# Performance work log

Measured on AMD Instinct MI355X. Metric: run time of the kernel, lower is better.

The kernel has to match this reference:

```python
import jax, jax.numpy as jnp
import numpy as np

EMBED = 1024
HEADS = 16
HEAD_DIM = EMBED // HEADS
LN_EPS = 1e-5


def setup_inputs() -> dict:
    key = jax.random.key(0)
    ks = jax.random.split(key, 12)
    B, LQ, LK = 2, 2048, 2048
    s = 1.0 / np.sqrt(EMBED)
    inp = {
        "query_seq": jax.random.normal(ks[0], (B, LQ, EMBED), jnp.float32),
        "key_value_seq": jax.random.normal(ks[1], (B, LK, EMBED), jnp.float32),
        "prompt_size": 0,
        "Wq": jax.random.normal(ks[2], (EMBED, EMBED), jnp.float32) * s,
        "bq": jnp.zeros((EMBED,), jnp.float32),
        "Wk": jax.random.normal(ks[3], (EMBED, EMBED), jnp.float32) * s,
        "bk": jnp.zeros((EMBED,), jnp.float32),
        "Wv": jax.random.normal(ks[4], (EMBED, EMBED), jnp.float32) * s,
        "bv": jnp.zeros((EMBED,), jnp.float32),
        "Wo": jax.random.normal(ks[5], (EMBED, EMBED), jnp.float32) * s,
        "bo": jnp.zeros((EMBED,), jnp.float32),
        "ln_gamma": jnp.ones((EMBED,), jnp.float32),
        "ln_beta": jnp.zeros((EMBED,), jnp.float32),
    }
    return inp


def _split_heads(x):
    B, L, _ = x.shape
    return x.reshape(B, L, HEADS, HEAD_DIM).transpose(0, 2, 1, 3)  # [B,H,L,Dh]


def reference(query_seq, key_value_seq, prompt_size, Wq, bq, Wk, bk, Wv, bv, Wo, bo, ln_gamma, ln_beta):
    # projections (torch nn.Linear: x @ W.T + b)
    q = _split_heads(query_seq @ Wq.T + bq)
    k = _split_heads(key_value_seq @ Wk.T + bk)
    v = _split_heads(key_value_seq @ Wv.T + bv)
    # naive attention: full score matrix, softmax over keys
    scores = jnp.einsum("bhqd,bhkd->bhqk", q, k) / np.sqrt(HEAD_DIM).astype(np.float32)
    attn = jax.nn.softmax(scores, axis=-1)
    ctx = jnp.einsum("bhqk,bhkd->bhqd", attn, v)
    B, H, LQ, Dh = ctx.shape
    ctx = ctx.transpose(0, 2, 1, 3).reshape(B, LQ, H * Dh)
    out = ctx @ Wo.T + bo
    # residual + LayerNorm
    x = out + query_seq
    mu = jnp.mean(x, axis=-1, keepdims=True)
    var = jnp.var(x, axis=-1, keepdims=True)
    return (x - mu) * jax.lax.rsqrt(var + LN_EPS) * ln_gamma + ln_beta
```

## Files before the change

kernel.cpp:

```cpp
#include <hip/hip_runtime.h>

typedef unsigned short u16;
typedef unsigned int u32;
typedef __attribute__((ext_vector_type(8))) __bf16 bf16x8;
typedef __attribute__((ext_vector_type(4))) short short4v;
typedef __attribute__((ext_vector_type(4))) float f32x4;
typedef __attribute__((ext_vector_type(16))) float f32x16;

#define EMBED 1024
#define NB 2
#define LQ 2048
#define HEADS 16
#define DH 64
#define QSCALE 0.18033688011112042f

__device__ __forceinline__ u16 f2bf(float f) {
  u32 u = __float_as_uint(f);
  u32 r = (u + 0x7FFFu + ((u >> 16) & 1u)) >> 16;
  return (u16)r;
}

__device__ __forceinline__ void glds16(const void* g, void* l) {
  __builtin_amdgcn_global_load_lds((const __attribute__((address_space(1))) void*)g,
                                   (__attribute__((address_space(3))) void*)l, 16, 0, 0);
}

__device__ __forceinline__ f32x4 mfma16(bf16x8 a, bf16x8 b, f32x4 c) {
  return __builtin_amdgcn_mfma_f32_16x16x32_bf16(a, b, c, 0, 0, 0);
}
__device__ __forceinline__ f32x16 mfma32(bf16x8 a, bf16x8 b, f32x16 c) {
  return __builtin_amdgcn_mfma_f32_32x32x16_bf16(a, b, c, 0, 0, 0);
}
__device__ __forceinline__ f32x16 mfma32x8(short4v a, short4v b, f32x16 c) {
  return __builtin_amdgcn_mfma_f32_32x32x8bf16_1k(a, b, c, 0, 0, 0);
}

__device__ __forceinline__ u32 packbf(float a, float b) {
  return __builtin_amdgcn_perm(__float_as_uint(b), __float_as_uint(a), 0x07060302u);
}

__global__ __launch_bounds__(256) void cast_kernel(
    const float* __restrict__ q, const float* __restrict__ kv,
    const float* __restrict__ wq, const float* __restrict__ wk,
    const float* __restrict__ wv, const float* __restrict__ wo,
    u16* __restrict__ qb, u16* __restrict__ kvb, u16* __restrict__ wqb,
    u16* __restrict__ wkb, u16* __restrict__ wvb, u16* __restrict__ wob) {
  int bid = blockIdx.x;
  const float* src;
  u16* dst;
  long base;
  if (bid < 2048) {
    src = q; dst = qb; base = (long)bid * 2048;
  } else if (bid < 4096) {
    src = kv; dst = kvb; base = (long)(bid - 2048) * 2048;
  } else {
    int wsel = (bid - 4096) >> 9;
    int wb = (bid - 4096) & 511;
    if (wsel == 0) { src = wq; dst = wqb; }
    else if (wsel == 1) { src = wk; dst = wkb; }
    else if (wsel == 2) { src = wv; dst = wvb; }
    else { src = wo; dst = wob; }
    base = (long)wb * 2048;
  }
  long e = base + (long)threadIdx.x * 8;
  float4 f0 = *(const float4*)(src + e);
  float4 f1 = *(const float4*)(src + e + 4);
  uint4 o;
  o.x = (u32)f2bf(f0.x) | ((u32)f2bf(f0.y) << 16);
  o.y = (u32)f2bf(f0.z) | ((u32)f2bf(f0.w) << 16);
  o.z = (u32)f2bf(f1.x) | ((u32)f2bf(f1.y) << 16);
  o.w = (u32)f2bf(f1.z) | ((u32)f2bf(f1.w) << 16);
  *(uint4*)(dst + e) = o;
}

template <int IT>
__device__ __forceinline__ void gemm_core(
    u16* As, u16* Bs, const u16* __restrict__ A, const u16* __restrict__ W,
    const float* __restrict__ bias, const float* __restrict__ resid,
    void* __restrict__ outp, int mode, int bx, int by) {
  const int K = EMBED;
  const int TM = IT * 32;
  const int tid = threadIdx.x;
  const int lane = tid & 63;
  const int wv = tid >> 6;
  const int wm = wv >> 1, wn = wv & 1;
  const int l16 = lane & 15, quad = lane >> 4;
  const long tile_m = (long)bx * TM;
  const long tile_n = (long)by * 128;

  f32x4 z4 = {0.f, 0.f, 0.f, 0.f};
  f32x4 acc[IT][4];
#pragma unroll
  for (int i = 0; i < IT; i++)
#pragma unroll
    for (int j = 0; j < 4; j++) acc[i][j] = z4;

  for (int k0 = 0; k0 < K; k0 += 64) {
#pragma unroll
    for (int it = 0; it < TM / 32; it++) {
      int lin = it * 256 + tid;
      int row = lin >> 3, cc = lin & 7;
      glds16(A + (tile_m + row) * K + k0 + ((cc ^ (row & 7)) << 3), As + lin * 8);
    }
#pragma unroll
    for (int it = 0; it < 4; it++) {
      int lin = it * 256 + tid;
      int row = lin >> 3, cc = lin & 7;
      glds16(W + (tile_n + row) * K + k0 + ((cc ^ (row & 7)) << 3), Bs + lin * 8);
    }
    __syncthreads();
    bf16x8 af[IT][2], bfr[4][2];
#pragma unroll
    for (int i = 0; i < IT; i++) {
      int row = wm * (IT * 16) + i * 16 + l16;
#pragma unroll
      for (int ki = 0; ki < 2; ki++)
        af[i][ki] = *(const bf16x8*)(As + row * 64 + (((ki * 4 + quad) ^ (row & 7)) << 3));
    }
#pragma unroll
    for (int j = 0; j < 4; j++) {
      int row = wn * 64 + j * 16 + l16;
#pragma unroll
      for (int ki = 0; ki < 2; ki++)
        bfr[j][ki] = *(const bf16x8*)(Bs + row * 64 + (((ki * 4 + quad) ^ (row & 7)) << 3));
    }
#pragma unroll
    for (int ki = 0; ki < 2; ki++)
#pragma unroll
      for (int i = 0; i < IT; i++)
#pragma unroll
        for (int j = 0; j < 4; j++) acc[i][j] = mfma16(af[i][ki], bfr[j][ki], acc[i][j]);
    __syncthreads();
  }

#pragma unroll
  for (int j = 0; j < 4; j++) {
    int gn = (int)tile_n + wn * 64 + j * 16 + l16;
    float bv = bias[gn];
#pragma unroll
    for (int i = 0; i < IT; i++) {
      long gm0 = tile_m + wm * (IT * 16) + i * 16 + quad * 4;
      if (mode == 3) {
#pragma unroll
        for (int r = 0; r < 4; r++) {
          long idx = (gm0 + r) * EMBED + gn;
          ((float*)outp)[idx] = acc[i][j][r] + bv + resid[idx];
        }
      } else if (mode == 2) {
        int b = (int)(gm0 >> 11), l = (int)(gm0 & 2047);
        int hh = gn >> 6, dh = gn & 63;
        uint2 pk;
        pk.x = (u32)f2bf(acc[i][j][0] + bv) | ((u32)f2bf(acc[i][j][1] + bv) << 16);
        pk.y = (u32)f2bf(acc[i][j][2] + bv) | ((u32)f2bf(acc[i][j][3] + bv) << 16);
        *(uint2*)((u16*)outp + (long)((b * HEADS + hh) * DH + dh) * LQ + l) = pk;
      } else {
#pragma unroll
        for (int r = 0; r < 4; r++) {
          long gm = gm0 + r;
          float v = acc[i][j][r] + bv;
          if (mode == 0) v *= QSCALE;
          int b = (int)(gm >> 11), l = (int)(gm & 2047);
          int hh = gn >> 6, dh = gn & 63;
          ((u16*)outp)[(long)((b * HEADS + hh) * LQ + l) * DH + dh] = f2bf(v);
        }
      }
    }
  }
}

__global__ __launch_bounds__(256) void qkv_kernel(
    const u16* __restrict__ qb, const u16* __restrict__ kvb,
    const u16* __restrict__ wqb, const u16* __restrict__ wkb, const u16* __restrict__ wvb,
    const float* __restrict__ bq, const float* __restrict__ bk, const float* __restrict__ bv,
    u16* __restrict__ Qh, u16* __restrict__ Kh, u16* __restrict__ Vt) {
  __shared__ u16 As[128 * 64];
  __shared__ u16 Bs[128 * 64];
  if (blockIdx.z == 0)      gemm_core<4>(As, Bs, qb,  wqb, bq, nullptr, Qh, 0, blockIdx.x, blockIdx.y);
  else if (blockIdx.z == 1) gemm_core<4>(As, Bs, kvb, wkb, bk, nullptr, Kh, 1, blockIdx.x, blockIdx.y);
  else                      gemm_core<4>(As, Bs, kvb, wvb, bv, nullptr, Vt, 2, blockIdx.x, blockIdx.y);
}

__global__ __launch_bounds__(256) void oproj_kernel(
    const u16* __restrict__ ctx, const u16* __restrict__ wob,
    const float* __restrict__ bo, const float* __restrict__ resid, float* __restrict__ out) {
  __shared__ u16 As[64 * 64];
  __shared__ u16 Bs[128 * 64];
  gemm_core<2>(As, Bs, ctx, wob, bo, resid, out, 3, blockIdx.x, blockIdx.y);
}

__global__ __launch_bounds__(256, 2) void attn_kernel(
    const u16* __restrict__ Qh, const u16* __restrict__ Kh,
    const u16* __restrict__ Vt, u16* __restrict__ ctx) {
  __shared__ u16 Qs[128 * 64];
  __shared__ u16 KVs[2][2][64 * 64];
  const int tid = threadIdx.x;
  const int lane = tid & 63;
  const int wv = tid >> 6;
  const int l32 = lane & 31, h = lane >> 5;
  const int qt = blockIdx.x, bh = blockIdx.y;
  const long qoff = (long)bh * (LQ * DH) + (long)qt * (128 * DH);
  const long koff = (long)bh * (LQ * DH);
  const long voff = (long)bh * (DH * LQ);
  const int qbase = wv * 32;

#pragma unroll
  for (int it = 0; it < 4; it++) {
    int lin = it * 256 + tid;
    int row = lin >> 3, cc = lin & 7;
    glds16(Qh + qoff + row * 64 + ((cc ^ (row & 7)) << 3), Qs + lin * 8);
  }
#pragma unroll
  for (int it = 0; it < 2; it++) {
    int lin = it * 256 + tid;
    int row = lin >> 3, cc = lin & 7;
    glds16(Kh + koff + (long)row * 64 + ((cc ^ (row & 7)) << 3), KVs[0][0] + lin * 8);
    glds16(Vt + voff + (long)row * LQ + ((cc ^ (row & 7)) << 3), KVs[0][1] + lin * 8);
  }
  __syncthreads();

  bf16x8 bq[4];
  {
    int row = qbase + l32;
#pragma unroll
    for (int ks = 0; ks < 4; ks++)
      bq[ks] = *(const bf16x8*)(Qs + row * 64 + (((ks * 2 + h) ^ (row & 7)) << 3));
  }

  f32x16 z16 = {0.f, 0.f, 0.f, 0.f, 0.f, 0.f, 0.f, 0.f,
                0.f, 0.f, 0.f, 0.f, 0.f, 0.f, 0.f, 0.f};
  f32x16 ot[2];
  ot[0] = z16;
  ot[1] = z16;
  float2 ls2 = {0.f, 0.f};

  for (int kt = 0; kt < 32; kt++) {
    const u16* Ks = KVs[kt & 1][0];
    const u16* Vts = KVs[kt & 1][1];
    if (kt + 1 < 32) {
      u16* Kn = (u16*)KVs[(kt + 1) & 1][0];
      u16* Vn = (u16*)KVs[(kt + 1) & 1][1];
#pragma unroll
      for (int it = 0; it < 2; it++) {
        int lin = it * 256 + tid;
        int row = lin >> 3, cc = lin & 7;
        glds16(Kh + koff + (long)((kt + 1) * 64 + row) * 64 + ((cc ^ (row & 7)) << 3), Kn + lin * 8);
        glds16(Vt + voff + (long)row * LQ + (kt + 1) * 64 + ((cc ^ (row & 7)) << 3), Vn + lin * 8);
      }
    }

    f32x16 st[2];
    st[0] = z16;
    st[1] = z16;
#pragma unroll
    for (int ks = 0; ks < 4; ks++) {
#pragma unroll
      for (int mt = 0; mt < 2; mt++) {
        int row = mt * 32 + l32;
        bf16x8 ak = *(const bf16x8*)(Ks + row * 64 + (((ks * 2 + h) ^ (row & 7)) << 3));
        st[mt] = mfma32(ak, bq[ks], st[mt]);
      }
    }

    uint2 pk[2][4];
#pragma unroll
    for (int mt = 0; mt < 2; mt++) {
#pragma unroll
      for (int g = 0; g < 4; g++) {
        float p0 = exp2f(st[mt][g * 4 + 0]);
        float p1 = exp2f(st[mt][g * 4 + 1]);
        float p2 = exp2f(st[mt][g * 4 + 2]);
        float p3 = exp2f(st[mt][g * 4 + 3]);
        float2 a = {p0, p1}, bb = {p2, p3};
        ls2.x += a.x + bb.x;
        ls2.y += a.y + bb.y;
        pk[mt][g].x = packbf(p0, p1);
        pk[mt][g].y = packbf(p2, p3);
      }
    }

#pragma unroll
    for (int t = 0; t < 8; t++) {
      short4v bp = *(short4v*)&pk[t >> 2][t & 3];
#pragma unroll
      for (int mt2 = 0; mt2 < 2; mt2++) {
        int row = mt2 * 32 + l32;
        short4v av = *(const short4v*)(Vts + row * 64 + (((t ^ (row & 7))) << 3) + 4 * h);
        ot[mt2] = mfma32x8(av, bp, ot[mt2]);
      }
    }
    __syncthreads();
  }

  float lsum = ls2.x + ls2.y;
  lsum += __shfl_xor(lsum, 32);
  float inv = 1.0f / lsum;

  const int b = bh >> 4, head = bh & 15;
  int qrow = qt * 128 + qbase + l32;
  long base = (long)(b * LQ + qrow) * EMBED + head * DH;
#pragma unroll
  for (int mt = 0; mt < 2; mt++) {
#pragma unroll
    for (int g = 0; g < 4; g++) {
      uint2 pkk;
      pkk.x = (u32)f2bf(ot[mt][g * 4 + 0] * inv) | ((u32)f2bf(ot[mt][g * 4 + 1] * inv) << 16);
      pkk.y = (u32)f2bf(ot[mt][g * 4 + 2] * inv) | ((u32)f2bf(ot[mt][g * 4 + 3] * inv) << 16);
      *(uint2*)(ctx + base + mt * 32 + g * 8 + 4 * h) = pkk;
    }
  }
}

__global__ __launch_bounds__(256) void ln_kernel(
    float* __restrict__ x, const float* __restrict__ gamma, const float* __restrict__ beta) {
  __shared__ float red[8];
  const int tid = threadIdx.x;
  const long row = blockIdx.x;
  float4 v = *(const float4*)(x + row * EMBED + tid * 4);
  float s = v.x + v.y + v.z + v.w;
  float sq = v.x * v.x + v.y * v.y + v.z * v.z + v.w * v.w;
#pragma unroll
  for (int off = 1; off < 64; off <<= 1) {
    s += __shfl_xor(s, off);
    sq += __shfl_xor(sq, off);
  }
  if ((tid & 63) == 0) {
    red[(tid >> 6) * 2] = s;
    red[(tid >> 6) * 2 + 1] = sq;
  }
  __syncthreads();
  s = red[0] + red[2] + red[4] + red[6];
  sq = red[1] + red[3] + red[5] + red[7];
  float mu = s * (1.f / EMBED);
  float var = sq * (1.f / EMBED) - mu * mu;
  float rstd = rsqrtf(var + 1e-5f);
  float4 g = *(const float4*)(gamma + tid * 4);
  float4 bt = *(const float4*)(beta + tid * 4);
  float4 ov;
  ov.x = (v.x - mu) * rstd * g.x + bt.x;
  ov.y = (v.y - mu) * rstd * g.y + bt.y;
  ov.z = (v.z - mu) * rstd * g.z + bt.z;
  ov.w = (v.w - mu) * rstd * g.w + bt.w;
  *(float4*)(x + row * EMBED + tid * 4) = ov;
}

extern "C" void kernel_launch(void* const* d_in, const int* in_sizes, int n_in,
                              void* d_out, int out_size, void* d_ws, size_t ws_size,
                              hipStream_t stream) {
  const float* q     = (const float*)d_in[0];
  const float* kv    = (const float*)d_in[1];
  const float* Wq    = (const float*)d_in[3];
  const float* bq    = (const float*)d_in[4];
  const float* Wk    = (const float*)d_in[5];
  const float* bk    = (const float*)d_in[6];
  const float* Wv    = (const float*)d_in[7];
  const float* bv    = (const float*)d_in[8];
  const float* Wo    = (const float*)d_in[9];
  const float* bo    = (const float*)d_in[10];
  const float* gamma = (const float*)d_in[11];
  const float* beta  = (const float*)d_in[12];

  char* ws = (char*)d_ws;
  u16* qb  = (u16*)(ws + (0l  << 20));
  u16* kvb = (u16*)(ws + (8l  << 20));
  u16* wqb = (u16*)(ws + (16l << 20));
  u16* wkb = (u16*)(ws + (18l << 20));
  u16* wvb = (u16*)(ws + (20l << 20));
  u16* wob = (u16*)(ws + (22l << 20));
  u16* Qh  = (u16*)(ws + (24l << 20));
  u16* Kh  = (u16*)(ws + (32l << 20));
  u16* Vt  = (u16*)(ws + (40l << 20));
  u16* ctx = (u16*)(ws + (48l << 20));
  float* out = (float*)d_out;

  cast_kernel<<<6144, 256, 0, stream>>>(q, kv, Wq, Wk, Wv, Wo, qb, kvb, wqb, wkb, wvb, wob);
  qkv_kernel<<<dim3(32, 8, 3), 256, 0, stream>>>(qb, kvb, wqb, wkb, wvb, bq, bk, bv, Qh, Kh, Vt);
  attn_kernel<<<dim3(16, 32), 256, 0, stream>>>(Qh, Kh, Vt, ctx);
  oproj_kernel<<<dim3(64, 8), 256, 0, stream>>>(ctx, wob, bo, q, out);
  ln_kernel<<<4096, 256, 0, stream>>>(out, gamma, beta);
}
```

Measured before the change: 241.6 us.

## Software-pipeline attention loop with triple-buffered KV and 32x32x16 PV MFMA

Restructures the attention main loop so the softmax of tile k-1 and its PV product run interleaved with the QK^T MFMAs for tile k, backed by a third KV LDS buffer and a two-tile prefetch distance. The PV step switches from the 32x32x8 MFMA to the 32x32x16 variant, using v_permlane32_swap to rearrange the packed probabilities into the wider operand layout. It also adds s_setprio around the MFMA blocks. The aim is to hide exp/convert latency and global-load latency behind matrix work and to halve the number of PV MFMA issues, at the cost of more LDS per block (occupancy risk with launch_bounds 256,2) and more live registers.

```diff
diff --git a/kernel.cpp b/kernel.cpp
--- a/kernel.cpp
+++ b/kernel.cpp
@@ -3,7 +3,6 @@
 typedef unsigned short u16;
 typedef unsigned int u32;
 typedef __attribute__((ext_vector_type(8))) __bf16 bf16x8;
-typedef __attribute__((ext_vector_type(4))) short short4v;
 typedef __attribute__((ext_vector_type(4))) float f32x4;
 typedef __attribute__((ext_vector_type(16))) float f32x16;
 
@@ -31,8 +30,9 @@
 __device__ __forceinline__ f32x16 mfma32(bf16x8 a, bf16x8 b, f32x16 c) {
   return __builtin_amdgcn_mfma_f32_32x32x16_bf16(a, b, c, 0, 0, 0);
 }
-__device__ __forceinline__ f32x16 mfma32x8(short4v a, short4v b, f32x16 c) {
-  return __builtin_amdgcn_mfma_f32_32x32x8bf16_1k(a, b, c, 0, 0, 0);
+
+__device__ __forceinline__ void pl32(u32& a, u32& b) {
+  asm("v_permlane32_swap_b32 %0, %1" : "+v"(a), "+v"(b));
 }
 
 __device__ __forceinline__ u32 packbf(float a, float b) {
@@ -192,7 +192,7 @@
     const u16* __restrict__ Qh, const u16* __restrict__ Kh,
     const u16* __restrict__ Vt, u16* __restrict__ ctx) {
   __shared__ u16 Qs[128 * 64];
-  __shared__ u16 KVs[2][2][64 * 64];
+  __shared__ u16 KVs[3][2][64 * 64];
   const int tid = threadIdx.x;
   const int lane = tid & 63;
   const int wv = tid >> 6;
@@ -203,19 +203,26 @@
   const long voff = (long)bh * (DH * LQ);
   const int qbase = wv * 32;
 
+  auto stage_kv = [&](int t, int r) {
+    u16* Kn = (u16*)KVs[r][0];
+    u16* Vn = (u16*)KVs[r][1];
+#pragma unroll
+    for (int it = 0; it < 2; it++) {
+      int lin = it * 256 + tid;
+      int row = lin >> 3, cc = lin & 7;
+      glds16(Kh + koff + (long)(t * 64 + row) * 64 + ((cc ^ (row & 7)) << 3), Kn + lin * 8);
+      glds16(Vt + voff + (long)row * LQ + t * 64 + ((cc ^ (row & 7)) << 3), Vn + lin * 8);
+    }
+  };
+
 #pragma unroll
   for (int it = 0; it < 4; it++) {
     int lin = it * 256 + tid;
     int row = lin >> 3, cc = lin & 7;
     glds16(Qh + qoff + row * 64 + ((cc ^ (row & 7)) << 3), Qs + lin * 8);
   }
-#pragma unroll
-  for (int it = 0; it < 2; it++) {
-    int lin = it * 256 + tid;
-    int row = lin >> 3, cc = lin & 7;
-    glds16(Kh + koff + (long)row * 64 + ((cc ^ (row & 7)) << 3), KVs[0][0] + lin * 8);
-    glds16(Vt + voff + (long)row * LQ + ((cc ^ (row & 7)) << 3), KVs[0][1] + lin * 8);
-  }
+  stage_kv(0, 0);
+  stage_kv(1, 1);
   __syncthreads();
 
   bf16x8 bq[4];
@@ -231,26 +238,14 @@
   f32x16 ot[2];
   ot[0] = z16;
   ot[1] = z16;
+  f32x16 st[2];
+  uint2 pk[2][4];
   float2 ls2 = {0.f, 0.f};
 
-  for (int kt = 0; kt < 32; kt++) {
-    const u16* Ks = KVs[kt & 1][0];
-    const u16* Vts = KVs[kt & 1][1];
-    if (kt + 1 < 32) {
-      u16* Kn = (u16*)KVs[(kt + 1) & 1][0];
-      u16* Vn = (u16*)KVs[(kt + 1) & 1][1];
-#pragma unroll
-      for (int it = 0; it < 2; it++) {
-        int lin = it * 256 + tid;
-        int row = lin >> 3, cc = lin & 7;
-        glds16(Kh + koff + (long)((kt + 1) * 64 + row) * 64 + ((cc ^ (row & 7)) << 3), Kn + lin * 8);
-        glds16(Vt + voff + (long)row * LQ + (kt + 1) * 64 + ((cc ^ (row & 7)) << 3), Vn + lin * 8);
-      }
-    }
-
-    f32x16 st[2];
+  auto do_S = [&](const u16* Ks) {
     st[0] = z16;
     st[1] = z16;
+    __builtin_amdgcn_s_setprio(1);
 #pragma unroll
     for (int ks = 0; ks < 4; ks++) {
 #pragma unroll
@@ -260,8 +255,10 @@
         st[mt] = mfma32(ak, bq[ks], st[mt]);
       }
     }
-
-    uint2 pk[2][4];
+    __builtin_amdgcn_s_setprio(0);
+  };
+
+  auto do_softmax = [&]() {
 #pragma unroll
     for (int mt = 0; mt < 2; mt++) {
 #pragma unroll
@@ -270,26 +267,53 @@
         float p1 = exp2f(st[mt][g * 4 + 1]);
         float p2 = exp2f(st[mt][g * 4 + 2]);
         float p3 = exp2f(st[mt][g * 4 + 3]);
-        float2 a = {p0, p1}, bb = {p2, p3};
-        ls2.x += a.x + bb.x;
-        ls2.y += a.y + bb.y;
+        ls2.x += p0 + p2;
+        ls2.y += p1 + p3;
         pk[mt][g].x = packbf(p0, p1);
         pk[mt][g].y = packbf(p2, p3);
       }
     }
-
-#pragma unroll
-    for (int t = 0; t < 8; t++) {
-      short4v bp = *(short4v*)&pk[t >> 2][t & 3];
+  };
+
+  auto do_PV = [&](const u16* Vts) {
+#pragma unroll
+    for (int s = 0; s < 4; s++) {
+      uint2 wa = pk[s >> 1][(s & 1) * 2];
+      uint2 wb = pk[s >> 1][(s & 1) * 2 + 1];
+      u32 a0 = wa.x, b0 = wb.x, a1 = wa.y, b1 = wb.y;
+      pl32(a0, b0);
+      pl32(a1, b1);
+      union { u32 u[4]; bf16x8 v; } bp;
+      bp.u[0] = a0;
+      bp.u[1] = a1;
+      bp.u[2] = b0;
+      bp.u[3] = b1;
+      __builtin_amdgcn_s_setprio(1);
 #pragma unroll
       for (int mt2 = 0; mt2 < 2; mt2++) {
         int row = mt2 * 32 + l32;
-        short4v av = *(const short4v*)(Vts + row * 64 + (((t ^ (row & 7))) << 3) + 4 * h);
-        ot[mt2] = mfma32x8(av, bp, ot[mt2]);
+        bf16x8 av = *(const bf16x8*)(Vts + row * 64 + ((((s << 1) + h) ^ (row & 7)) << 3));
+        ot[mt2] = mfma32(av, bp.v, ot[mt2]);
       }
-    }
+      __builtin_amdgcn_s_setprio(0);
+    }
+  };
+
+  do_S(KVs[0][0]);
+
+  int prv = 0, cur = 1, nxt = 2;
+  for (int kt = 1; kt < 32; kt++) {
+    if (kt + 1 < 32) stage_kv(kt + 1, nxt);
+    do_softmax();
+    do_S(KVs[cur][0]);
+    do_PV(KVs[prv][1]);
     __syncthreads();
-  }
+    prv = cur;
+    cur = nxt;
+    nxt = (nxt == 2) ? 0 : nxt + 1;
+  }
+  do_softmax();
+  do_PV(KVs[prv][1]);
 
   float lsum = ls2.x + ls2.y;
   lsum += __shfl_xor(lsum, 32);
```

New measurement: 234.5 us. -2.9%, faster.

## Software-pipeline attention loop with triple-buffered KV and wider PV MFMA

Applied to the files above, without the earlier changes.

The attention inner loop is restructured so each iteration runs the softmax of the previous tile, the QK^T MFMAs of the current tile and the PV MFMAs of the previous tile. K/V tiles are staged two ahead into a third LDS buffer. The PV product switches from the 32x32x8 MFMA to 32x32x16 by regrouping the probability registers with v_permlane32_swap, and s_setprio is raised around the MFMA blocks. The goal is to overlap exp/pack work with matrix ops and halve the PV MFMA count. The cost is more LDS per block and more live registers.

```diff
diff --git a/kernel.cpp b/kernel.cpp
--- a/kernel.cpp
+++ b/kernel.cpp
@@ -3,7 +3,6 @@
 typedef unsigned short u16;
 typedef unsigned int u32;
 typedef __attribute__((ext_vector_type(8))) __bf16 bf16x8;
-typedef __attribute__((ext_vector_type(4))) short short4v;
 typedef __attribute__((ext_vector_type(4))) float f32x4;
 typedef __attribute__((ext_vector_type(16))) float f32x16;
 
@@ -31,8 +30,9 @@
 __device__ __forceinline__ f32x16 mfma32(bf16x8 a, bf16x8 b, f32x16 c) {
   return __builtin_amdgcn_mfma_f32_32x32x16_bf16(a, b, c, 0, 0, 0);
 }
-__device__ __forceinline__ f32x16 mfma32x8(short4v a, short4v b, f32x16 c) {
-  return __builtin_amdgcn_mfma_f32_32x32x8bf16_1k(a, b, c, 0, 0, 0);
+
+__device__ __forceinline__ void pl32(u32& a, u32& b) {
+  asm("v_permlane32_swap_b32 %0, %1" : "+v"(a), "+v"(b));
 }
 
 __device__ __forceinline__ u32 packbf(float a, float b) {
@@ -192,7 +192,7 @@
     const u16* __restrict__ Qh, const u16* __restrict__ Kh,
     const u16* __restrict__ Vt, u16* __restrict__ ctx) {
   __shared__ u16 Qs[128 * 64];
-  __shared__ u16 KVs[2][2][64 * 64];
+  __shared__ u16 KVs[3][2][64 * 64];
   const int tid = threadIdx.x;
   const int lane = tid & 63;
   const int wv = tid >> 6;
@@ -203,19 +203,26 @@
   const long voff = (long)bh * (DH * LQ);
   const int qbase = wv * 32;
 
+#define STAGE_KV(t, N)                                                          \
+  do {                                                                          \
+    _Pragma("unroll") for (int it = 0; it < 2; it++) {                          \
+      int lin = it * 256 + tid;                                                 \
+      int row = lin >> 3, cc = lin & 7;                                         \
+      glds16(Kh + koff + (long)((t) * 64 + row) * 64 + ((cc ^ (row & 7)) << 3), \
+             &KVs[N][0][0] + lin * 8);                                          \
+      glds16(Vt + voff + (long)row * LQ + (t) * 64 + ((cc ^ (row & 7)) << 3),   \
+             &KVs[N][1][0] + lin * 8);                                          \
+    }                                                                           \
+  } while (0)
+
 #pragma unroll
   for (int it = 0; it < 4; it++) {
     int lin = it * 256 + tid;
     int row = lin >> 3, cc = lin & 7;
     glds16(Qh + qoff + row * 64 + ((cc ^ (row & 7)) << 3), Qs + lin * 8);
   }
-#pragma unroll
-  for (int it = 0; it < 2; it++) {
-    int lin = it * 256 + tid;
-    int row = lin >> 3, cc = lin & 7;
-    glds16(Kh + koff + (long)row * 64 + ((cc ^ (row & 7)) << 3), KVs[0][0] + lin * 8);
-    glds16(Vt + voff + (long)row * LQ + ((cc ^ (row & 7)) << 3), KVs[0][1] + lin * 8);
-  }
+  STAGE_KV(0, 0);
+  STAGE_KV(1, 1);
   __syncthreads();
 
   bf16x8 bq[4];
@@ -231,65 +238,91 @@
   f32x16 ot[2];
   ot[0] = z16;
   ot[1] = z16;
+  f32x16 st[2];
+  uint2 pk[2][4];
   float2 ls2 = {0.f, 0.f};
 
-  for (int kt = 0; kt < 32; kt++) {
-    const u16* Ks = KVs[kt & 1][0];
-    const u16* Vts = KVs[kt & 1][1];
-    if (kt + 1 < 32) {
-      u16* Kn = (u16*)KVs[(kt + 1) & 1][0];
-      u16* Vn = (u16*)KVs[(kt + 1) & 1][1];
-#pragma unroll
-      for (int it = 0; it < 2; it++) {
-        int lin = it * 256 + tid;
-        int row = lin >> 3, cc = lin & 7;
-        glds16(Kh + koff + (long)((kt + 1) * 64 + row) * 64 + ((cc ^ (row & 7)) << 3), Kn + lin * 8);
-        glds16(Vt + voff + (long)row * LQ + (kt + 1) * 64 + ((cc ^ (row & 7)) << 3), Vn + lin * 8);
-      }
-    }
-
-    f32x16 st[2];
-    st[0] = z16;
-    st[1] = z16;
-#pragma unroll
-    for (int ks = 0; ks < 4; ks++) {
-#pragma unroll
-      for (int mt = 0; mt < 2; mt++) {
-        int row = mt * 32 + l32;
-        bf16x8 ak = *(const bf16x8*)(Ks + row * 64 + (((ks * 2 + h) ^ (row & 7)) << 3));
-        st[mt] = mfma32(ak, bq[ks], st[mt]);
-      }
-    }
-
-    uint2 pk[2][4];
-#pragma unroll
-    for (int mt = 0; mt < 2; mt++) {
-#pragma unroll
-      for (int g = 0; g < 4; g++) {
-        float p0 = exp2f(st[mt][g * 4 + 0]);
-        float p1 = exp2f(st[mt][g * 4 + 1]);
-        float p2 = exp2f(st[mt][g * 4 + 2]);
-        float p3 = exp2f(st[mt][g * 4 + 3]);
-        float2 a = {p0, p1}, bb = {p2, p3};
-        ls2.x += a.x + bb.x;
-        ls2.y += a.y + bb.y;
-        pk[mt][g].x = packbf(p0, p1);
-        pk[mt][g].y = packbf(p2, p3);
-      }
-    }
-
-#pragma unroll
-    for (int t = 0; t < 8; t++) {
-      short4v bp = *(short4v*)&pk[t >> 2][t & 3];
-#pragma unroll
-      for (int mt2 = 0; mt2 < 2; mt2++) {
-        int row = mt2 * 32 + l32;
-        short4v av = *(const short4v*)(Vts + row * 64 + (((t ^ (row & 7))) << 3) + 4 * h);
-        ot[mt2] = mfma32x8(av, bp, ot[mt2]);
-      }
-    }
-    __syncthreads();
-  }
+#define DO_S(C)                                                                  \
+  do {                                                                           \
+    st[0] = z16;                                                                 \
+    st[1] = z16;                                                                 \
+    __builtin_amdgcn_s_setprio(1);                                               \
+    _Pragma("unroll") for (int ks = 0; ks < 4; ks++) {                           \
+      _Pragma("unroll") for (int mt = 0; mt < 2; mt++) {                         \
+        int row = mt * 32 + l32;                                                 \
+        bf16x8 ak = *(const bf16x8*)(&KVs[C][0][0] + row * 64 +                  \
+                                     (((ks * 2 + h) ^ (row & 7)) << 3));         \
+        st[mt] = mfma32(ak, bq[ks], st[mt]);                                     \
+      }                                                                          \
+    }                                                                            \
+    __builtin_amdgcn_s_setprio(0);                                               \
+  } while (0)
+
+#define DO_SM()                                                                  \
+  do {                                                                           \
+    _Pragma("unroll") for (int mt = 0; mt < 2; mt++) {                           \
+      _Pragma("unroll") for (int g = 0; g < 4; g++) {                            \
+        float p0 = __builtin_amdgcn_exp2f(st[mt][g * 4 + 0]);                    \
+        float p1 = __builtin_amdgcn_exp2f(st[mt][g * 4 + 1]);                    \
+        float p2 = __builtin_amdgcn_exp2f(st[mt][g * 4 + 2]);                    \
+        float p3 = __builtin_amdgcn_exp2f(st[mt][g * 4 + 3]);                    \
+        ls2.x += p0 + p2;                                                        \
+        ls2.y += p1 + p3;                                                        \
+        pk[mt][g].x = packbf(p0, p1);                                            \
+        pk[mt][g].y = packbf(p2, p3);                                            \
+      }                                                                          \
+    }                                                                            \
+  } while (0)
+
+#define DO_PV(P)                                                                 \
+  do {                                                                           \
+    _Pragma("unroll") for (int s = 0; s < 4; s++) {                              \
+      uint2 wa = pk[s >> 1][(s & 1) * 2];                                        \
+      uint2 wb = pk[s >> 1][(s & 1) * 2 + 1];                                    \
+      u32 a0 = wa.x, b0 = wb.x, a1 = wa.y, b1 = wb.y;                            \
+      pl32(a0, b0);                                                              \
+      pl32(a1, b1);                                                              \
+      union { u32 u[4]; bf16x8 v; } bp;                                          \
+      bp.u[0] = a0;                                                              \
+      bp.u[1] = a1;                                                              \
+      bp.u[2] = b0;                                                              \
+      bp.u[3] = b1;                                                              \
+      __builtin_amdgcn_s_setprio(1);                                             \
+      _Pragma("unroll") for (int mt2 = 0; mt2 < 2; mt2++) {                      \
+        int row = mt2 * 32 + l32;                                                \
+        bf16x8 av = *(const bf16x8*)(&KVs[P][1][0] + row * 64 +                  \
+                                     ((((s << 1) + h) ^ (row & 7)) << 3));       \
+        ot[mt2] = mfma32(av, bp.v, ot[mt2]);                                     \
+      }                                                                          \
+      __builtin_amdgcn_s_setprio(0);                                             \
+    }                                                                            \
+  } while (0)
+
+#define AITER(kt, P, C, N)                                                       \
+  do {                                                                           \
+    if ((kt) + 1 < 32) STAGE_KV((kt) + 1, N);                                    \
+    DO_SM();                                                                     \
+    DO_S(C);                                                                     \
+    DO_PV(P);                                                                    \
+    __syncthreads();                                                             \
+  } while (0)
+
+  DO_S(0);
+
+  AITER(1, 0, 1, 2);
+  for (int k0 = 2; k0 < 32; k0 += 3) {
+    AITER(k0, 1, 2, 0);
+    AITER(k0 + 1, 2, 0, 1);
+    AITER(k0 + 2, 0, 1, 2);
+  }
+  DO_SM();
+  DO_PV(1);
+
+#undef STAGE_KV
+#undef DO_S
+#undef DO_SM
+#undef DO_PV
+#undef AITER
 
   float lsum = ls2.x + ls2.y;
   lsum += __shfl_xor(lsum, 32);
```

Result: faster. 222.4 us (-8.0%).
